# Performance work log

Hardware: AMD Instinct MI355X
Metric: run time of the kernel (lower is better)

Reference implementation:

```python
import jax, jax.numpy as jnp
import numpy as np

EPS = 1e-7
N, L, BATCH = 512, 2, 128
N_IPF = 10


def setup_inputs() -> dict:
    key = jax.random.key(0)
    k1, k2, k3, k4 = jax.random.split(key, 4)
    return {
        "x": jax.random.randint(k1, (BATCH, N), 0, L, dtype=jnp.int32),
        "W": jax.random.normal(k2, (N, N), dtype=jnp.float32),
        "V_compress": jax.random.normal(k3, (N, L), dtype=jnp.float32),
        "E_compress": jax.random.normal(k4, (N, N, L, L), dtype=jnp.float32),
    }


def _moat_forward(W, V_compress, E_compress, x):
    n, l = V_compress.shape
    # marginals / joints
    V = jax.nn.softmax(V_compress, axis=1)              # (n, l)
    E = jnp.exp(E_compress)                              # (n, n, l, l)
    E = E / E.sum(axis=(-2, -1), keepdims=True)

    # 10-step Sinkhorn / IPF projection onto marginals V
    A_b = V[:, None, :, None]                            # (n, 1, l, 1)
    B_b = V[None, :, None, :]                            # (1, n, 1, l)
    for _ in range(N_IPF):
        row_marg = E.sum(axis=3, keepdims=True) + EPS    # (n, n, l, 1)
        col_marg = E.sum(axis=2, keepdims=True) + EPS    # (n, n, 1, l)
        E = E * (A_b / row_marg)
        E = E * (B_b / col_marg)
        E = E / (E.sum(axis=(-2, -1), keepdims=True) + EPS)

    # zero the diagonal (i == j) pairwise joints, clamp
    E = E * (1.0 - jnp.eye(n, dtype=E.dtype))[:, :, None, None]
    E = jnp.clip(E, 0.0, 1.0)

    # symmetric edge-weight matrix from strictly-lower-triangular sigmoid(W)
    Wm = jax.nn.sigmoid(W)
    Wm = jnp.tril(Wm, k=-1)
    Wm = Wm.T + Wm                                       # (n, n), zero diag
    L_0 = -Wm + jnp.diag(Wm.sum(axis=1))                 # graph Laplacian

    idx = jnp.arange(n)
    # Pr[b, i] = V[i, x[b, i]]
    Pr = V[idx[None, :], x]                              # (batch, n)
    # P[b, i, j] = E[i, j, x[b, i], x[b, j]]
    P = E[idx[None, :, None], idx[None, None, :], x[:, :, None], x[:, None, :]]  # (batch, n, n)
    P = P / (Pr[:, :, None] * Pr[:, None, :])

    WP = Wm[None, :, :] * P                              # (batch, n, n)
    Lb = -WP + jax.vmap(jnp.diag)(WP.sum(axis=2))        # batched Laplacian

    # matrix-tree theorem: logdet of the (n-1, n-1) principal minor
    _, logdet_L = jnp.linalg.slogdet(Lb[:, 1:, 1:])
    _, logdet_L0 = jnp.linalg.slogdet(L_0[1:, 1:])
    return jnp.log(Pr).sum(axis=1) + logdet_L - logdet_L0  # (batch,)


def reference(x, W, V_compress, E_compress):
    return _moat_forward(W, V_compress, E_compress, x)
```

## Files before the change

### kernel.cpp

```cpp
#include <hip/hip_runtime.h>
#include <hip/hip_bf16.h>
#include <math.h>

#define NDIM 512
#define NB   128
#define NMAT 129
#define EPSF 1e-7f
#define MS  ((size_t)262144)
#define PSTR ((size_t)524288)

#define OFF_E   ((size_t)0)
#define OFF_WM  ((size_t)1048576)
#define OFF_IPR ((size_t)1310720)
#define OFF_LPR ((size_t)1376256)
#define OFF_LD  ((size_t)1376384)
#define OFF_MAT ((size_t)1377792)

__device__ __forceinline__ float rdlane(float v, int l) {
  return __uint_as_float((unsigned)__builtin_amdgcn_readlane((int)__float_as_uint(v), l));
}

__global__ __launch_bounds__(256) void k_prep(const float* __restrict__ W, const float* __restrict__ Vc,
                                              const float* __restrict__ Ec, float* __restrict__ Wm,
                                              float* __restrict__ E2) {
  int idx = blockIdx.x * 256 + threadIdx.x;
  int i = idx >> 9, j = idx & 511;
  float wv = 0.f;
  if (i > j)      wv = 1.f / (1.f + expf(-W[i*NDIM + j]));
  else if (i < j) wv = 1.f / (1.f + expf(-W[j*NDIM + i]));
  Wm[idx] = wv;
  float vi0 = Vc[2*i], vi1 = Vc[2*i+1];
  float mi = fmaxf(vi0, vi1);
  float ei0 = expf(vi0 - mi), ei1 = expf(vi1 - mi);
  float si = ei0 + ei1;
  float A0 = ei0 / si, A1 = ei1 / si;
  float vj0 = Vc[2*j], vj1 = Vc[2*j+1];
  float mj = fmaxf(vj0, vj1);
  float ej0 = expf(vj0 - mj), ej1 = expf(vj1 - mj);
  float sj = ej0 + ej1;
  float B0 = ej0 / sj, B1 = ej1 / sj;
  float4 ec = reinterpret_cast<const float4*>(Ec)[idx];
  float e00 = expf(ec.x), e01 = expf(ec.y), e10 = expf(ec.z), e11 = expf(ec.w);
  float s = e00 + e01 + e10 + e11;
  float inv = 1.f / s;
  e00 *= inv; e01 *= inv; e10 *= inv; e11 *= inv;
  for (int t = 0; t < 10; ++t) {
    float rm0 = e00 + e01 + EPSF, rm1 = e10 + e11 + EPSF;
    float cm0 = e00 + e10 + EPSF, cm1 = e01 + e11 + EPSF;
    float f0 = A0 / rm0, f1 = A1 / rm1;
    e00 *= f0; e01 *= f0; e10 *= f1; e11 *= f1;
    float g0 = B0 / cm0, g1 = B1 / cm1;
    e00 *= g0; e10 *= g0; e01 *= g1; e11 *= g1;
    float ss = e00 + e01 + e10 + e11 + EPSF;
    float iv = 1.f / ss;
    e00 *= iv; e01 *= iv; e10 *= iv; e11 *= iv;
  }
  if (i == j) { e00 = 0.f; e01 = 0.f; e10 = 0.f; e11 = 0.f; }
  e00 = fminf(fmaxf(e00, 0.f), 1.f);
  e01 = fminf(fmaxf(e01, 0.f), 1.f);
  e10 = fminf(fmaxf(e10, 0.f), 1.f);
  e11 = fminf(fmaxf(e11, 0.f), 1.f);
  reinterpret_cast<float2*>(E2)[idx]        = make_float2(e00, e01);
  reinterpret_cast<float2*>(E2 + PSTR)[idx] = make_float2(e10, e11);
}

__global__ __launch_bounds__(256) void k_Pr(const int* __restrict__ x, const float* __restrict__ Vc,
                                            float* __restrict__ invPr, float* __restrict__ logPr) {
  const int b = blockIdx.x;
  const int tid = threadIdx.x;
  float acc = 0.f;
  for (int ii = tid; ii < NDIM; ii += 256) {
    const int xv = x[b*NDIM + ii];
    float v0 = Vc[2*ii], v1 = Vc[2*ii+1];
    float mx = fmaxf(v0, v1);
    float e0 = expf(v0 - mx), e1 = expf(v1 - mx);
    float s = e0 + e1;
    const float p = xv ? (e1 / s) : (e0 / s);
    invPr[b*NDIM + ii] = 1.f / p;
    acc += logf(p);
  }
  for (int off = 32; off > 0; off >>= 1) acc += __shfl_down(acc, off, 64);
  __shared__ float sw[4];
  if ((tid & 63) == 0) sw[tid >> 6] = acc;
  __syncthreads();
  if (tid == 0) logPr[b] = sw[0] + sw[1] + sw[2] + sw[3];
}

__global__ __launch_bounds__(512) void k_build(const int* __restrict__ x, const float* __restrict__ E2,
                                               const float* __restrict__ Wm, const float* __restrict__ invPr,
                                               float* __restrict__ Mall) {
  const int b = blockIdx.x;
  const int i = blockIdx.y*8 + (threadIdx.x >> 6);
  const int lane = threadIdx.x & 63;
  const int j0 = lane << 3;

  const float4 w0 = *(const float4*)(Wm + (size_t)i*NDIM + j0);
  const float4 w1 = *(const float4*)(Wm + (size_t)i*NDIM + j0 + 4);
  float wp[8];
  if (b < NB) {
    const int   xi   = x[b*NDIM + i];
    const float ipri = invPr[b*NDIM + i];
    const int4  xa = *(const int4*)(x + b*NDIM + j0);
    const int4  xb = *(const int4*)(x + b*NDIM + j0 + 4);
    const float4 pa = *(const float4*)(invPr + b*NDIM + j0);
    const float4 pb = *(const float4*)(invPr + b*NDIM + j0 + 4);
    const float* pl = E2 + (size_t)xi*PSTR + ((size_t)i*NDIM + j0)*2;
    const float4 ea = *(const float4*)(pl);
    const float4 eb = *(const float4*)(pl + 4);
    const float4 ec = *(const float4*)(pl + 8);
    const float4 ed = *(const float4*)(pl + 12);
    wp[0] = w0.x * (xa.x ? ea.y : ea.x) * pa.x;
    wp[1] = w0.y * (xa.y ? ea.w : ea.z) * pa.y;
    wp[2] = w0.z * (xa.z ? eb.y : eb.x) * pa.z;
    wp[3] = w0.w * (xa.w ? eb.w : eb.z) * pa.w;
    wp[4] = w1.x * (xb.x ? ec.y : ec.x) * pb.x;
    wp[5] = w1.y * (xb.y ? ec.w : ec.z) * pb.y;
    wp[6] = w1.z * (xb.z ? ed.y : ed.x) * pb.z;
    wp[7] = w1.w * (xb.w ? ed.w : ed.z) * pb.w;
    #pragma unroll
    for (int k = 0; k < 8; ++k) wp[k] *= ipri;
  } else {
    wp[0]=w0.x; wp[1]=w0.y; wp[2]=w0.z; wp[3]=w0.w;
    wp[4]=w1.x; wp[5]=w1.y; wp[6]=w1.z; wp[7]=w1.w;
  }
  float s = ((wp[0]+wp[1])+(wp[2]+wp[3])) + ((wp[4]+wp[5])+(wp[6]+wp[7]));
  #pragma unroll
  for (int off = 32; off > 0; off >>= 1) s += __shfl_xor(s, off, 64);

  float o[8];
  #pragma unroll
  for (int k = 0; k < 8; ++k) o[k] = -wp[k];
  if (i == 0) {
    #pragma unroll
    for (int k = 0; k < 8; ++k) o[k] = 0.f;
    if (lane == 0) o[0] = 1.f;
  } else {
    if (lane == 0) o[0] = 0.f;
    #pragma unroll
    for (int k = 0; k < 8; ++k)
      if (j0 + k == i) o[k] = s;
  }
  float* dst = Mall + (size_t)b*MS + (size_t)i*NDIM + j0;
  *(float4*)(dst)   = make_float4(o[0],o[1],o[2],o[3]);
  *(float4*)(dst+4) = make_float4(o[4],o[5],o[6],o[7]);
}

template<int KK>
struct WFact {
  static __device__ __forceinline__ void run(float (&a)[64], const int lane,
                                             float& mypiv, float& myrec) {
    const float piv = rdlane(a[KK], KK);
    const float rec = 1.0f / piv;
    if (lane == KK) { mypiv = piv; myrec = rec; }
    if (lane > KK) {
      const float l = a[KK] * rec;
      a[KK] = l;
      #pragma unroll
      for (int c = KK + 1; c < 64; ++c)
        a[c] -= l * rdlane(a[c], KK);
    }
    WFact<KK + 1>::run(a, lane, mypiv, myrec);
  }
};
template<>
struct WFact<64> {
  static __device__ __forceinline__ void run(float (&)[64], int, float&, float&) {}
};

template<int C>
struct SolveStep {
  static __device__ __forceinline__ void run(float (&a)[64], const float (*T)[68]) {
    float acc = a[C];
    #pragma unroll
    for (int p = 0; p < C; ++p)
      acc -= a[p] * T[C][p];
    a[C] = acc * T[C][66];
    SolveStep<C + 1>::run(a, T);
  }
};
template<>
struct SolveStep<64> {
  static __device__ __forceinline__ void run(float (&)[64], const float (*)[68]) {}
};

__global__ __launch_bounds__(512) void k_panelA(float* __restrict__ Mall,
                                                float* __restrict__ logdets, int k0) {
  const int b = blockIdx.x;
  float* __restrict__ M = Mall + (size_t)b*MS;
  const int t = threadIdx.x;
  const int m = NDIM - k0;
  const int mrem = m - 64;
  __shared__ float T[64][68];

  float a[64];
  if (t < m) {
    const float* row = M + (size_t)(k0+t)*NDIM + k0;
    #pragma unroll
    for (int c4 = 0; c4 < 16; ++c4) {
      float4 v = *(const float4*)(row + c4*4);
      a[c4*4+0]=v.x; a[c4*4+1]=v.y; a[c4*4+2]=v.z; a[c4*4+3]=v.w;
    }
  }
  if (t < 64) {
    float mypiv = 1.f, myrec = 1.f;
    WFact<0>::run(a, t, mypiv, myrec);
    #pragma unroll
    for (int c = 0; c < 64; ++c) T[c][t] = a[c];
    T[t][66] = myrec;
    float v = logf(fabsf(mypiv));
    #pragma unroll
    for (int off = 32; off > 0; off >>= 1) v += __shfl_down(v, off, 64);
    if (t == 0) logdets[b] = (k0 == 0) ? v : (logdets[b] + v);
  }
  __syncthreads();

  if (mrem > 0) {
    if (t >= 64 && t < m) {
      SolveStep<0>::run(a, T);
      float* row = M + (size_t)(k0+t)*NDIM + k0;
      #pragma unroll
      for (int c4 = 0; c4 < 16; ++c4)
        *(float4*)(row + c4*4) = make_float4(a[c4*4],a[c4*4+1],a[c4*4+2],a[c4*4+3]);
    }
    if (t < mrem) {
      const int col = k0 + 64 + t;
      float u[64];
      #pragma unroll
      for (int r = 0; r < 64; ++r) u[r] = M[(size_t)(k0+r)*NDIM + col];
      #pragma unroll
      for (int p = 0; p < 63; ++p) {
        const float lv = u[p];
        #pragma unroll
        for (int kk = p+1; kk < 64; ++kk) u[kk] -= T[p][kk] * lv;
      }
      #pragma unroll
      for (int r = 1; r < 64; ++r) M[(size_t)(k0+r)*NDIM + col] = u[r];
    }
  }
}

__global__ __launch_bounds__(256, 4) void k_strip(float* __restrict__ Mall, int k0) {
  const int b = blockIdx.x;
  float* __restrict__ M = Mall + (size_t)b*MS;
  __shared__ float As[64][68];
  __shared__ float Bs[64][68];
  const int tid = threadIdx.x;
  const int tx = tid & 15, ty = tid >> 4;
  const int rowbase = 64 + blockIdx.y*64;
  #pragma unroll
  for (int i = 0; i < 4; ++i) {
    const int q = tid + 256*i, qr = q >> 4, qf = q & 15;
    const float4 va = *(const float4*)&M[(size_t)(k0+rowbase+qr)*NDIM + k0 + qf*4];
    As[qf*4+0][qr]=va.x; As[qf*4+1][qr]=va.y; As[qf*4+2][qr]=va.z; As[qf*4+3][qr]=va.w;
    *(float4*)&Bs[qr][qf*4] = *(const float4*)&M[(size_t)(k0+qr)*NDIM + (k0+64) + qf*4];
  }
  float* Crow = M + (size_t)(k0+rowbase+ty*4)*NDIM + (k0+64+tx*4);
  float4 c0 = *(float4*)(Crow + 0*NDIM);
  float4 c1 = *(float4*)(Crow + 1*NDIM);
  float4 c2 = *(float4*)(Crow + 2*NDIM);
  float4 c3 = *(float4*)(Crow + 3*NDIM);
  __syncthreads();
  #pragma unroll
  for (int p = 0; p < 64; ++p) {
    const float4 av = *(const float4*)&As[p][ty*4];
    const float4 bv = *(const float4*)&Bs[p][tx*4];
    c0.x -= av.x*bv.x; c0.y -= av.x*bv.y; c0.z -= av.x*bv.z; c0.w -= av.x*bv.w;
    c1.x -= av.y*bv.x; c1.y -= av.y*bv.y; c1.z -= av.y*bv.z; c1.w -= av.y*bv.w;
    c2.x -= av.z*bv.x; c2.y -= av.z*bv.y; c2.z -= av.z*bv.z; c2.w -= av.z*bv.w;
    c3.x -= av.w*bv.x; c3.y -= av.w*bv.y; c3.z -= av.w*bv.z; c3.w -= av.w*bv.w;
  }
  *(float4*)(Crow + 0*NDIM) = c0;
  *(float4*)(Crow + 1*NDIM) = c1;
  *(float4*)(Crow + 2*NDIM) = c2;
  *(float4*)(Crow + 3*NDIM) = c3;
}

__global__ __launch_bounds__(512) void k_panelB(float* __restrict__ Mall,
                                                float* __restrict__ logdets, int k0, int ncols) {
  const int b = blockIdx.x;
  float* __restrict__ M = Mall + (size_t)b*MS;
  const int t = threadIdx.x;
  const int m = NDIM - k0;
  __shared__ float T[64][68];
  __shared__ float Ls2[64][68];

  float s[64];
  if (t < 64) {
    const float* row = M + (size_t)(k0+64+t)*NDIM + (k0+64);
    #pragma unroll
    for (int c4 = 0; c4 < 16; ++c4) {
      float4 v = *(const float4*)(row + c4*4);
      s[c4*4+0]=v.x; s[c4*4+1]=v.y; s[c4*4+2]=v.z; s[c4*4+3]=v.w;
    }
  } else if (t < 128) {
    const int r = t - 64;
    const float* row = M + (size_t)(k0+64+r)*NDIM + k0;
    #pragma unroll
    for (int c = 0; c < 64; ++c) Ls2[c][r] = row[c];
  } else if (t < m) {
    const float* row = M + (size_t)(k0+t)*NDIM + (k0+64);
    #pragma unroll
    for (int c4 = 0; c4 < 16; ++c4) {
      float4 v = *(const float4*)(row + c4*4);
      s[c4*4+0]=v.x; s[c4*4+1]=v.y; s[c4*4+2]=v.z; s[c4*4+3]=v.w;
    }
  }

  if (t < 64) {
    float mypiv = 1.f, myrec = 1.f;
    WFact<0>::run(s, t, mypiv, myrec);
    #pragma unroll
    for (int c = 0; c < 64; ++c) T[c][t] = s[c];
    T[t][66] = myrec;
    float v = logf(fabsf(mypiv));
    #pragma unroll
    for (int off = 32; off > 0; off >>= 1) v += __shfl_down(v, off, 64);
    if (t == 0) logdets[b] += v;
  }
  __syncthreads();

  if (t >= 128 && t < m) {
    SolveStep<0>::run(s, T);
    float* row = M + (size_t)(k0+t)*NDIM + (k0+64);
    #pragma unroll
    for (int c4 = 0; c4 < 16; ++c4)
      *(float4*)(row + c4*4) = make_float4(s[c4*4],s[c4*4+1],s[c4*4+2],s[c4*4+3]);
  }

  if (t < ncols) {
    const int col = k0 + 128 + t;
    float u[64];
    #pragma unroll
    for (int r = 0; r < 64; ++r) u[r] = M[(size_t)(k0+64+r)*NDIM + col];
    #pragma unroll
    for (int p = 0; p < 64; ++p) {
      const float up = M[(size_t)(k0+p)*NDIM + col];
      #pragma unroll
      for (int r = 0; r < 64; ++r) u[r] -= Ls2[p][r] * up;
    }
    #pragma unroll
    for (int p = 0; p < 63; ++p) {
      const float lv = u[p];
      #pragma unroll
      for (int kk = p+1; kk < 64; ++kk) u[kk] -= T[p][kk] * lv;
    }
    #pragma unroll
    for (int r = 0; r < 64; ++r) M[(size_t)(k0+64+r)*NDIM + col] = u[r];
  }
}

__global__ __launch_bounds__(256, 4) void k_gemm2(float* __restrict__ Mall, int k0) {
  const int b = blockIdx.x;
  float* __restrict__ M = Mall + (size_t)b*MS;
  __shared__ float As[64][68];
  __shared__ float Bs[64][68];
  const int tid = threadIdx.x;
  const int tx = tid & 15, ty = tid >> 4;
  const int rowbase = 128 + blockIdx.y*64;
  const int colbase = 128 + blockIdx.z*64;
  float* Crow = M + (size_t)(k0+rowbase+ty*4)*NDIM + (k0+colbase+tx*4);
  float4 c0 = *(float4*)(Crow + 0*NDIM);
  float4 c1 = *(float4*)(Crow + 1*NDIM);
  float4 c2 = *(float4*)(Crow + 2*NDIM);
  float4 c3 = *(float4*)(Crow + 3*NDIM);
  #pragma unroll
  for (int i = 0; i < 4; ++i) {
    const int q = tid + 256*i, qr = q >> 4, qf = q & 15;
    const float4 va = *(const float4*)&M[(size_t)(k0+rowbase+qr)*NDIM + k0 + qf*4];
    As[qf*4+0][qr]=va.x; As[qf*4+1][qr]=va.y; As[qf*4+2][qr]=va.z; As[qf*4+3][qr]=va.w;
    *(float4*)&Bs[qr][qf*4] = *(const float4*)&M[(size_t)(k0+qr)*NDIM + (k0+colbase) + qf*4];
  }
  __syncthreads();
  float4 ra[4], rb[4];
  #pragma unroll
  for (int i = 0; i < 4; ++i) {
    const int q = tid + 256*i, qr = q >> 4, qf = q & 15;
    ra[i] = *(const float4*)&M[(size_t)(k0+rowbase+qr)*NDIM + k0 + 64 + qf*4];
    rb[i] = *(const float4*)&M[(size_t)(k0+64+qr)*NDIM + (k0+colbase) + qf*4];
  }
  #pragma unroll
  for (int p = 0; p < 64; ++p) {
    const float4 av = *(const float4*)&As[p][ty*4];
    const float4 bv = *(const float4*)&Bs[p][tx*4];
    c0.x -= av.x*bv.x; c0.y -= av.x*bv.y; c0.z -= av.x*bv.z; c0.w -= av.x*bv.w;
    c1.x -= av.y*bv.x; c1.y -= av.y*bv.y; c1.z -= av.y*bv.z; c1.w -= av.y*bv.w;
    c2.x -= av.z*bv.x; c2.y -= av.z*bv.y; c2.z -= av.z*bv.z; c2.w -= av.z*bv.w;
    c3.x -= av.w*bv.x; c3.y -= av.w*bv.y; c3.z -= av.w*bv.z; c3.w -= av.w*bv.w;
  }
  __syncthreads();
  #pragma unroll
  for (int i = 0; i < 4; ++i) {
    const int q = tid + 256*i, qr = q >> 4, qf = q & 15;
    As[qf*4+0][qr]=ra[i].x; As[qf*4+1][qr]=ra[i].y; As[qf*4+2][qr]=ra[i].z; As[qf*4+3][qr]=ra[i].w;
    *(float4*)&Bs[qr][qf*4] = rb[i];
  }
  __syncthreads();
  #pragma unroll
  for (int p = 0; p < 64; ++p) {
    const float4 av = *(const float4*)&As[p][ty*4];
    const float4 bv = *(const float4*)&Bs[p][tx*4];
    c0.x -= av.x*bv.x; c0.y -= av.x*bv.y; c0.z -= av.x*bv.z; c0.w -= av.x*bv.w;
    c1.x -= av.y*bv.x; c1.y -= av.y*bv.y; c1.z -= av.y*bv.z; c1.w -= av.y*bv.w;
    c2.x -= av.z*bv.x; c2.y -= av.z*bv.y; c2.z -= av.z*bv.z; c2.w -= av.z*bv.w;
    c3.x -= av.w*bv.x; c3.y -= av.w*bv.y; c3.z -= av.w*bv.z; c3.w -= av.w*bv.w;
  }
  *(float4*)(Crow + 0*NDIM) = c0;
  *(float4*)(Crow + 1*NDIM) = c1;
  *(float4*)(Crow + 2*NDIM) = c2;
  *(float4*)(Crow + 3*NDIM) = c3;
}

__global__ void k_final(const float* __restrict__ logPr, const float* __restrict__ logdets,
                        float* __restrict__ out) {
  int t = threadIdx.x;
  if (t < NB) out[t] = logPr[t] + logdets[t] - logdets[NB];
}

extern "C" void kernel_launch(void* const* d_in, const int* in_sizes, int n_in,
                              void* d_out, int out_size, void* d_ws, size_t ws_size,
                              hipStream_t stream) {
  const int*   x  = (const int*)  d_in[0];
  const float* W  = (const float*)d_in[1];
  const float* Vc = (const float*)d_in[2];
  const float* Ec = (const float*)d_in[3];
  float* out = (float*)d_out;
  float* ws  = (float*)d_ws;
  (void)in_sizes; (void)n_in; (void)out_size; (void)ws_size;

  float* Mat = ws + OFF_MAT;
  float* Ld  = ws + OFF_LD;

  k_prep<<<1024, 256, 0, stream>>>(W, Vc, Ec, ws + OFF_WM, ws + OFF_E);
  k_Pr  <<<NB,   256, 0, stream>>>(x, Vc, ws + OFF_IPR, ws + OFF_LPR);
  dim3 gb(NMAT, 64);
  k_build<<<gb, 512, 0, stream>>>(x, ws + OFF_E, ws + OFF_WM, ws + OFF_IPR, Mat);

  for (int S = 0; S < 4; ++S) {
    const int k0 = S*128;
    const int m = NDIM - k0;
    const int ncols = m - 128;
    k_panelA<<<NMAT, 512, 0, stream>>>(Mat, Ld, k0);
    dim3 gs(NMAT, (m - 64)/64);
    k_strip<<<gs, 256, 0, stream>>>(Mat, k0);
    k_panelB<<<NMAT, 512, 0, stream>>>(Mat, Ld, k0, ncols);
    if (ncols > 0) {
      const int nt = ncols/64;
      dim3 gg(NMAT, nt, nt);
      k_gemm2<<<gg, 256, 0, stream>>>(Mat, k0);
    }
  }
  k_final<<<1, 128, 0, stream>>>(ws + OFF_LPR, Ld, out);
}
```

Measured before the change: 672.9 us.

## Split panel kernels across 8 sub-blocks and store L panel transposed

```diff
diff --git a/kernel.cpp b/kernel.cpp
--- a/kernel.cpp
+++ b/kernel.cpp
@@ -8,6 +8,7 @@
 #define EPSF 1e-7f
 #define MS  ((size_t)262144)
 #define PSTR ((size_t)524288)
+#define LTS2 ((size_t)65536)
 
 #define OFF_E   ((size_t)0)
 #define OFF_WM  ((size_t)1048576)
@@ -15,6 +16,7 @@
 #define OFF_LPR ((size_t)1376256)
 #define OFF_LD  ((size_t)1376384)
 #define OFF_MAT ((size_t)1377792)
+#define OFF_LT  ((size_t)(OFF_MAT + (size_t)NMAT*MS))
 
 __device__ __forceinline__ float rdlane(float v, int l) {
   return __uint_as_float((unsigned)__builtin_amdgcn_readlane((int)__float_as_uint(v), l));
@@ -183,25 +185,26 @@
   static __device__ __forceinline__ void run(float (&)[64], const float (*)[68]) {}
 };
 
-__global__ __launch_bounds__(512) void k_panelA(float* __restrict__ Mall,
+__global__ __launch_bounds__(128) void k_panelA(float* __restrict__ Mall, float* __restrict__ LtAll,
                                                 float* __restrict__ logdets, int k0) {
   const int b = blockIdx.x;
-  float* __restrict__ M = Mall + (size_t)b*MS;
+  const int sub = blockIdx.y;
+  float* __restrict__ M  = Mall  + (size_t)b*MS;
+  float* __restrict__ Lt = LtAll + (size_t)b*LTS2;
   const int t = threadIdx.x;
   const int m = NDIM - k0;
   const int mrem = m - 64;
+  const int rs = (mrem + 7) >> 3;
   __shared__ float T[64][68];
 
   float a[64];
-  if (t < m) {
+  if (t < 64) {
     const float* row = M + (size_t)(k0+t)*NDIM + k0;
     #pragma unroll
     for (int c4 = 0; c4 < 16; ++c4) {
       float4 v = *(const float4*)(row + c4*4);
       a[c4*4+0]=v.x; a[c4*4+1]=v.y; a[c4*4+2]=v.z; a[c4*4+3]=v.w;
     }
-  }
-  if (t < 64) {
     float mypiv = 1.f, myrec = 1.f;
     WFact<0>::run(a, t, mypiv, myrec);
     #pragma unroll
@@ -210,48 +213,59 @@
     float v = logf(fabsf(mypiv));
     #pragma unroll
     for (int off = 32; off > 0; off >>= 1) v += __shfl_down(v, off, 64);
-    if (t == 0) logdets[b] = (k0 == 0) ? v : (logdets[b] + v);
+    if (sub == 0 && t == 0) logdets[b] = (k0 == 0) ? v : (logdets[b] + v);
   }
   __syncthreads();
 
   if (mrem > 0) {
-    if (t >= 64 && t < m) {
-      SolveStep<0>::run(a, T);
-      float* row = M + (size_t)(k0+t)*NDIM + k0;
-      #pragma unroll
-      for (int c4 = 0; c4 < 16; ++c4)
-        *(float4*)(row + c4*4) = make_float4(a[c4*4],a[c4*4+1],a[c4*4+2],a[c4*4+3]);
-    }
-    if (t < mrem) {
-      const int col = k0 + 64 + t;
-      float u[64];
-      #pragma unroll
-      for (int r = 0; r < 64; ++r) u[r] = M[(size_t)(k0+r)*NDIM + col];
-      #pragma unroll
-      for (int p = 0; p < 63; ++p) {
-        const float lv = u[p];
-        #pragma unroll
-        for (int kk = p+1; kk < 64; ++kk) u[kk] -= T[p][kk] * lv;
+    if (t >= 64) {
+      const int idx = sub*rs + (t - 64);
+      if ((t - 64) < rs && idx < mrem) {
+        const int gr = k0 + 64 + idx;
+        const float* row = M + (size_t)gr*NDIM + k0;
+        #pragma unroll
+        for (int c4 = 0; c4 < 16; ++c4) {
+          float4 v = *(const float4*)(row + c4*4);
+          a[c4*4+0]=v.x; a[c4*4+1]=v.y; a[c4*4+2]=v.z; a[c4*4+3]=v.w;
+        }
+        SolveStep<0>::run(a, T);
+        #pragma unroll
+        for (int c = 0; c < 64; ++c) Lt[(size_t)c*NDIM + gr] = a[c];
       }
-      #pragma unroll
-      for (int r = 1; r < 64; ++r) M[(size_t)(k0+r)*NDIM + col] = u[r];
-    }
-  }
-}
-
-__global__ __launch_bounds__(256, 4) void k_strip(float* __restrict__ Mall, int k0) {
-  const int b = blockIdx.x;
-  float* __restrict__ M = Mall + (size_t)b*MS;
+    } else {
+      const int idx = sub*rs + t;
+      if (t < rs && idx < mrem) {
+        const int col = k0 + 64 + idx;
+        float u[64];
+        #pragma unroll
+        for (int r = 0; r < 64; ++r) u[r] = M[(size_t)(k0+r)*NDIM + col];
+        #pragma unroll
+        for (int p = 0; p < 63; ++p) {
+          const float lv = u[p];
+          #pragma unroll
+          for (int kk = p+1; kk < 64; ++kk) u[kk] -= T[p][kk] * lv;
+        }
+        #pragma unroll
+        for (int r = 1; r < 64; ++r) M[(size_t)(k0+r)*NDIM + col] = u[r];
+      }
+    }
+  }
+}
+
+__global__ __launch_bounds__(256, 4) void k_strip(float* __restrict__ Mall, const float* __restrict__ LtAll,
+                                                  int k0) {
+  const int b = blockIdx.y;
+  float* __restrict__ M  = Mall  + (size_t)b*MS;
+  const float* __restrict__ Lt = LtAll + (size_t)b*LTS2;
   __shared__ float As[64][68];
   __shared__ float Bs[64][68];
   const int tid = threadIdx.x;
   const int tx = tid & 15, ty = tid >> 4;
-  const int rowbase = 64 + blockIdx.y*64;
+  const int rowbase = 64 + blockIdx.x*64;
   #pragma unroll
   for (int i = 0; i < 4; ++i) {
     const int q = tid + 256*i, qr = q >> 4, qf = q & 15;
-    const float4 va = *(const float4*)&M[(size_t)(k0+rowbase+qr)*NDIM + k0 + qf*4];
-    As[qf*4+0][qr]=va.x; As[qf*4+1][qr]=va.y; As[qf*4+2][qr]=va.z; As[qf*4+3][qr]=va.w;
+    *(float4*)&As[qr][qf*4] = *(const float4*)&Lt[(size_t)qr*NDIM + (k0+rowbase) + qf*4];
     *(float4*)&Bs[qr][qf*4] = *(const float4*)&M[(size_t)(k0+qr)*NDIM + (k0+64) + qf*4];
   }
   float* Crow = M + (size_t)(k0+rowbase+ty*4)*NDIM + (k0+64+tx*4);
@@ -275,12 +289,14 @@
   *(float4*)(Crow + 3*NDIM) = c3;
 }
 
-__global__ __launch_bounds__(512) void k_panelB(float* __restrict__ Mall,
+__global__ __launch_bounds__(128) void k_panelB(float* __restrict__ Mall, float* __restrict__ LtAll,
                                                 float* __restrict__ logdets, int k0, int ncols) {
   const int b = blockIdx.x;
-  float* __restrict__ M = Mall + (size_t)b*MS;
+  const int sub = blockIdx.y;
+  float* __restrict__ M  = Mall  + (size_t)b*MS;
+  float* __restrict__ Lt = LtAll + (size_t)b*LTS2;
   const int t = threadIdx.x;
-  const int m = NDIM - k0;
+  const int rs = (ncols + 7) >> 3;
   __shared__ float T[64][68];
   __shared__ float Ls2[64][68];
 
@@ -292,21 +308,6 @@
       float4 v = *(const float4*)(row + c4*4);
       s[c4*4+0]=v.x; s[c4*4+1]=v.y; s[c4*4+2]=v.z; s[c4*4+3]=v.w;
     }
-  } else if (t < 128) {
-    const int r = t - 64;
-    const float* row = M + (size_t)(k0+64+r)*NDIM + k0;
-    #pragma unroll
-    for (int c = 0; c < 64; ++c) Ls2[c][r] = row[c];
-  } else if (t < m) {
-    const float* row = M + (size_t)(k0+t)*NDIM + (k0+64);
-    #pragma unroll
-    for (int c4 = 0; c4 < 16; ++c4) {
-      float4 v = *(const float4*)(row + c4*4);
-      s[c4*4+0]=v.x; s[c4*4+1]=v.y; s[c4*4+2]=v.z; s[c4*4+3]=v.w;
-    }
-  }
-
-  if (t < 64) {
     float mypiv = 1.f, myrec = 1.f;
     WFact<0>::run(s, t, mypiv, myrec);
     #pragma unroll
@@ -315,49 +316,66 @@
     float v = logf(fabsf(mypiv));
     #pragma unroll
     for (int off = 32; off > 0; off >>= 1) v += __shfl_down(v, off, 64);
-    if (t == 0) logdets[b] += v;
-  }
-  __syncthreads();
-
-  if (t >= 128 && t < m) {
-    SolveStep<0>::run(s, T);
-    float* row = M + (size_t)(k0+t)*NDIM + (k0+64);
-    #pragma unroll
-    for (int c4 = 0; c4 < 16; ++c4)
-      *(float4*)(row + c4*4) = make_float4(s[c4*4],s[c4*4+1],s[c4*4+2],s[c4*4+3]);
-  }
-
-  if (t < ncols) {
-    const int col = k0 + 128 + t;
-    float u[64];
-    #pragma unroll
-    for (int r = 0; r < 64; ++r) u[r] = M[(size_t)(k0+64+r)*NDIM + col];
-    #pragma unroll
-    for (int p = 0; p < 64; ++p) {
-      const float up = M[(size_t)(k0+p)*NDIM + col];
-      #pragma unroll
-      for (int r = 0; r < 64; ++r) u[r] -= Ls2[p][r] * up;
-    }
-    #pragma unroll
-    for (int p = 0; p < 63; ++p) {
-      const float lv = u[p];
-      #pragma unroll
-      for (int kk = p+1; kk < 64; ++kk) u[kk] -= T[p][kk] * lv;
-    }
-    #pragma unroll
-    for (int r = 0; r < 64; ++r) M[(size_t)(k0+64+r)*NDIM + col] = u[r];
-  }
-}
-
-__global__ __launch_bounds__(256, 4) void k_gemm2(float* __restrict__ Mall, int k0) {
-  const int b = blockIdx.x;
-  float* __restrict__ M = Mall + (size_t)b*MS;
+    if (sub == 0 && t == 0) logdets[b] += v;
+  } else {
+    const int r = t - 64;
+    #pragma unroll
+    for (int c = 0; c < 64; ++c) Ls2[c][r] = Lt[(size_t)c*NDIM + (k0+64+r)];
+  }
+  __syncthreads();
+
+  if (ncols > 0) {
+    if (t >= 64) {
+      const int idx = sub*rs + (t - 64);
+      if ((t - 64) < rs && idx < ncols) {
+        const int gr = k0 + 128 + idx;
+        const float* row = M + (size_t)gr*NDIM + (k0+64);
+        #pragma unroll
+        for (int c4 = 0; c4 < 16; ++c4) {
+          float4 v = *(const float4*)(row + c4*4);
+          s[c4*4+0]=v.x; s[c4*4+1]=v.y; s[c4*4+2]=v.z; s[c4*4+3]=v.w;
+        }
+        SolveStep<0>::run(s, T);
+        #pragma unroll
+        for (int c = 0; c < 64; ++c) Lt[(size_t)(64+c)*NDIM + gr] = s[c];
+      }
+    } else {
+      const int idx = sub*rs + t;
+      if (t < rs && idx < ncols) {
+        const int col = k0 + 128 + idx;
+        float u[64];
+        #pragma unroll
+        for (int r = 0; r < 64; ++r) u[r] = M[(size_t)(k0+64+r)*NDIM + col];
+        #pragma unroll
+        for (int p = 0; p < 64; ++p) {
+          const float up = M[(size_t)(k0+p)*NDIM + col];
+          #pragma unroll
+          for (int r = 0; r < 64; ++r) u[r] -= Ls2[p][r] * up;
+        }
+        #pragma unroll
+        for (int p = 0; p < 63; ++p) {
+          const float lv = u[p];
+          #pragma unroll
+          for (int kk = p+1; kk < 64; ++kk) u[kk] -= T[p][kk] * lv;
+        }
+        #pragma unroll
+        for (int r = 0; r < 64; ++r) M[(size_t)(k0+64+r)*NDIM + col] = u[r];
+      }
+    }
+  }
+}
+
+__global__ __launch_bounds__(256, 4) void k_gemm2(float* __restrict__ Mall, const float* __restrict__ LtAll,
+                                                  int k0) {
+  const int b = blockIdx.z;
+  float* __restrict__ M  = Mall  + (size_t)b*MS;
+  const float* __restrict__ Lt = LtAll + (size_t)b*LTS2;
   __shared__ float As[64][68];
   __shared__ float Bs[64][68];
   const int tid = threadIdx.x;
   const int tx = tid & 15, ty = tid >> 4;
-  const int rowbase = 128 + blockIdx.y*64;
-  const int colbase = 128 + blockIdx.z*64;
+  const int rowbase = 128 + blockIdx.x*64;
+  const int colbase = 128 + blockIdx.y*64;
   float* Crow = M + (size_t)(k0+rowbase+ty*4)*NDIM + (k0+colbase+tx*4);
   float4 c0 = *(float4*)(Crow + 0*NDIM);
   float4 c1 = *(float4*)(Crow + 1*NDIM);
@@ -366,8 +384,7 @@
   #pragma unroll
   for (int i = 0; i < 4; ++i) {
     const int q = tid + 256*i, qr = q >> 4, qf = q & 15;
-    const float4 va = *(const float4*)&M[(size_t)(k0+rowbase+qr)*NDIM + k0 + qf*4];
-    As[qf*4+0][qr]=va.x; As[qf*4+1][qr]=va.y; As[qf*4+2][qr]=va.z; As[qf*4+3][qr]=va.w;
+    *(float4*)&As[qr][qf*4] = *(const float4*)&Lt[(size_t)qr*NDIM + (k0+rowbase) + qf*4];
     *(float4*)&Bs[qr][qf*4] = *(const float4*)&M[(size_t)(k0+qr)*NDIM + (k0+colbase) + qf*4];
   }
   __syncthreads();
@@ -375,7 +392,7 @@
   #pragma unroll
   for (int i = 0; i < 4; ++i) {
     const int q = tid + 256*i, qr = q >> 4, qf = q & 15;
-    ra[i] = *(const float4*)&M[(size_t)(k0+rowbase+qr)*NDIM + k0 + 64 + qf*4];
+    ra[i] = *(const float4*)&Lt[(size_t)(64+qr)*NDIM + (k0+rowbase) + qf*4];
     rb[i] = *(const float4*)&M[(size_t)(k0+64+qr)*NDIM + (k0+colbase) + qf*4];
   }
   #pragma unroll
@@ -391,7 +408,7 @@
   #pragma unroll
   for (int i = 0; i < 4; ++i) {
     const int q = tid + 256*i, qr = q >> 4, qf = q & 15;
-    As[qf*4+0][qr]=ra[i].x; As[qf*4+1][qr]=ra[i].y; As[qf*4+2][qr]=ra[i].z; As[qf*4+3][qr]=ra[i].w;
+    *(float4*)&As[qr][qf*4] = ra[i];
     *(float4*)&Bs[qr][qf*4] = rb[i];
   }
   __syncthreads();
@@ -428,6 +445,7 @@
   (void)in_sizes; (void)n_in; (void)out_size; (void)ws_size;
 
   float* Mat = ws + OFF_MAT;
+  float* Lt  = ws + OFF_LT;
   float* Ld  = ws + OFF_LD;
 
   k_prep<<<1024, 256, 0, stream>>>(W, Vc, Ec, ws + OFF_WM, ws + OFF_E);
@@ -438,15 +456,18 @@
   for (int S = 0; S < 4; ++S) {
     const int k0 = S*128;
     const int m = NDIM - k0;
+    const int mrem = m - 64;
     const int ncols = m - 128;
-    k_panelA<<<NMAT, 512, 0, stream>>>(Mat, Ld, k0);
-    dim3 gs(NMAT, (m - 64)/64);
-    k_strip<<<gs, 256, 0, stream>>>(Mat, k0);
-    k_panelB<<<NMAT, 512, 0, stream>>>(Mat, Ld, k0, ncols);
+    dim3 gpa(NMAT, 8);
+    k_panelA<<<gpa, 128, 0, stream>>>(Mat, Lt, Ld, k0);
+    dim3 gs(mrem/64, NMAT);
+    k_strip<<<gs, 256, 0, stream>>>(Mat, Lt, k0);
+    dim3 gpb(NMAT, (ncols > 0) ? 8 : 1);
+    k_panelB<<<gpb, 128, 0, stream>>>(Mat, Lt, Ld, k0, ncols);
     if (ncols > 0) {
       const int nt = ncols/64;
-      dim3 gg(NMAT, nt, nt);
-      k_gemm2<<<gg, 256, 0, stream>>>(Mat, k0);
+      dim3 gg(nt, nt, NMAT);
+      k_gemm2<<<gg, 256, 0, stream>>>(Mat, Lt, k0);
     }
   }
   k_final<<<1, 128, 0, stream>>>(ws + OFF_LPR, Ld, out);
```

Measured after the change: 886.6 us. 1.32x slower.
